# Kernel optimization log

Measured on AMD Instinct MI355X. Metric: run time of the kernel, lower is better.

## Reference

```python
import jax, jax.numpy as jnp
import numpy as np

B, S, V, E, H = 256, 256, 128, 512, 512
D1, D2, NT, NE = 1024, 512, 12, 5
BN_EPS = 1e-5


def setup_inputs() -> dict:
    key = jax.random.key(0)
    ks = jax.random.split(key, 12)
    p = lambda k, shape: jax.random.normal(k, shape, jnp.float32) * 0.05
    return dict(
        smiles=jax.random.randint(ks[0], (B, S), 0, V),
        emb=p(ks[1], (V, E)),
        W_ih0=p(ks[2], (3 * H, E)), W_hh0=p(ks[3], (3 * H, H)),
        b_ih0=jnp.zeros(3 * H), b_hh0=jnp.zeros(3 * H),
        W_ih1=p(ks[4], (3 * H, H)), W_hh1=p(ks[5], (3 * H, H)),
        b_ih1=jnp.zeros(3 * H), b_hh1=jnp.zeros(3 * H),
        Wd1=p(ks[6], (D1, H)), bd1=jnp.zeros(D1), g1=jnp.ones(D1), beta1=jnp.zeros(D1),
        Wd2=p(ks[7], (D2, D1)), bd2=jnp.zeros(D2), g2=jnp.ones(D2), beta2=jnp.zeros(D2),
        We=p(ks[8], (NE, NT, D2)), be=jnp.zeros((NE, NT)),
    )


def _gru_layer(x, W_ih, W_hh, b_ih, b_hh):
    """x: [B,S,Din]. Returns (h_T [B,H], seq [B,S,H]). Torch GRUCell math."""
    xi = jnp.einsum('bsd,gd->bsg', x, W_ih) + b_ih  # precompute input gates [B,S,3H]
    h0 = jnp.zeros((x.shape[0], W_hh.shape[0] // 3), x.dtype)

    def step(h, xi_t):
        hh = h @ W_hh.T + b_hh
        xr, xz, xn = jnp.split(xi_t, 3, axis=-1)
        hr, hz, hn = jnp.split(hh, 3, axis=-1)
        r = jax.nn.sigmoid(xr + hr)
        z = jax.nn.sigmoid(xz + hz)
        n = jnp.tanh(xn + r * hn)
        h_new = (1.0 - z) * n + z * h
        return h_new, h_new

    hT, hs = jax.lax.scan(step, h0, jnp.swapaxes(xi, 0, 1))
    return hT, jnp.swapaxes(hs, 0, 1)


def _bn(x, g, b):
    m = x.mean(0)
    v = x.var(0)
    return g * (x - m) * jax.lax.rsqrt(v + BN_EPS) + b


def reference(smiles, emb, W_ih0, W_hh0, b_ih0, b_hh0, W_ih1, W_hh1, b_ih1, b_hh1,
              Wd1, bd1, g1, beta1, Wd2, bd2, g2, beta2, We, be):
    x = emb[smiles]                                   # [B,S,E]
    _, seq = _gru_layer(x, W_ih0, W_hh0, b_ih0, b_hh0)  # [B,S,H]
    hT, _ = _gru_layer(seq, W_ih1, W_hh1, b_ih1, b_hh1)  # final hidden [B,H]
    h = jax.nn.relu(_bn(hT @ Wd1.T + bd1, g1, beta1))   # dense_0: Linear->BN->ReLU
    h = jax.nn.relu(_bn(h @ Wd2.T + bd2, g2, beta2))    # dense_1
    scores = jnp.einsum('bd,etd->bet', h, We) + be      # [B,NE,NT]
    return jax.nn.sigmoid(scores.mean(axis=1))          # ensemble 'score': sigmoid(mean)
```

## Files before the change

kernel.cpp:

```cpp
#include <hip/hip_runtime.h>
#include <stdint.h>

#define WS_TABLE0   0
#define WS_WHH0B    786432
#define WS_WIH1B    2359296
#define WS_WHH1B    3932160
#define WS_WD1B     5505024
#define WS_WD2B     6553600
#define WS_WM       7602176
#define WS_BM       7626752
#define WS_H0B      7627008
#define WS_H1B      8151296
#define WS_Y1       8675584
#define WS_X1B      9724160
#define WS_Y2       10248448
#define WS_X2B      10772736
#define WS_BAR      11034880

typedef __attribute__((ext_vector_type(8))) short bf16x8;
typedef __attribute__((ext_vector_type(4))) float f32x4;

__device__ __forceinline__ unsigned short f2bf(float f) {
  uint32_t u = __builtin_bit_cast(uint32_t, f);
  u += 0x7fffu + ((u >> 16) & 1u);
  return (unsigned short)(u >> 16);
}
__device__ __forceinline__ float bf2f(unsigned short s) {
  uint32_t u = ((uint32_t)s) << 16;
  return __builtin_bit_cast(float, u);
}
__device__ __forceinline__ float sigf(float x) { return 1.f / (1.f + __expf(-x)); }
__device__ __forceinline__ float tanhs(float x) {
  x = fminf(fmaxf(x, -10.f), 10.f);
  float e = __expf(2.f * x);
  return (e - 1.f) / (e + 1.f);
}

__device__ __forceinline__ unsigned long long pack4(float a, float b, float c, float d) {
  return (unsigned long long)f2bf(a) | ((unsigned long long)f2bf(b) << 16) |
         ((unsigned long long)f2bf(c) << 32) | ((unsigned long long)f2bf(d) << 48);
}

__device__ __forceinline__ void st_wt64(unsigned long long* p, unsigned long long v) {
  __hip_atomic_store(p, v, __ATOMIC_RELAXED, __HIP_MEMORY_SCOPE_AGENT);
}

__device__ __forceinline__ void gbar(int* bar, int expected) {
  __syncthreads();
  if (threadIdx.x == 0) {
    __threadfence();
    int g0 = __hip_atomic_load(bar + 1, __ATOMIC_RELAXED, __HIP_MEMORY_SCOPE_AGENT);
    int a = __hip_atomic_fetch_add(bar, 1, __ATOMIC_ACQ_REL, __HIP_MEMORY_SCOPE_AGENT);
    if (a == expected - 1) {
      __hip_atomic_store(bar, 0, __ATOMIC_RELAXED, __HIP_MEMORY_SCOPE_AGENT);
      __hip_atomic_fetch_add(bar + 1, 1, __ATOMIC_RELEASE, __HIP_MEMORY_SCOPE_AGENT);
    } else {
      while (__hip_atomic_load(bar + 1, __ATOMIC_RELAXED, __HIP_MEMORY_SCOPE_AGENT) == g0) {
        __builtin_amdgcn_s_sleep(1);
      }
    }
    __threadfence();
  }
  __syncthreads();
}

__global__ void k_zero(uint4* p, int n16) {
  int i = blockIdx.x * 256 + threadIdx.x;
  if (i < n16) p[i] = make_uint4(0u, 0u, 0u, 0u);
}

__global__ void k_cvt(const float* __restrict__ src, unsigned short* __restrict__ dst, int n) {
  int i = (blockIdx.x * 256 + threadIdx.x) * 4;
  if (i < n) {
    float4 v = *(const float4*)(src + i);
    dst[i + 0] = f2bf(v.x);
    dst[i + 1] = f2bf(v.y);
    dst[i + 2] = f2bf(v.z);
    dst[i + 3] = f2bf(v.w);
  }
}

__global__ void k_table(const float* __restrict__ emb, const float* __restrict__ Wih0,
                        const float* __restrict__ bih0, float* __restrict__ table) {
  __shared__ float e[512];
  int v = blockIdx.x;
  for (int i = threadIdx.x; i < 512; i += 256) e[i] = emb[v * 512 + i];
  __syncthreads();
  for (int cidx = threadIdx.x; cidx < 1536; cidx += 256) {
    const float* w = Wih0 + (size_t)cidx * 512;
    float s = 0.f;
    #pragma unroll 4
    for (int k = 0; k < 512; k += 4) {
      float4 w4 = *(const float4*)(w + k);
      s += w4.x * e[k] + w4.y * e[k + 1] + w4.z * e[k + 2] + w4.w * e[k + 3];
    }
    table[(size_t)v * 1536 + cidx] = s + bih0[cidx];
  }
}

__global__ void k_wm(const float* __restrict__ We, const float* __restrict__ be,
                     float* __restrict__ Wm, float* __restrict__ bm) {
  int i = blockIdx.x * 256 + threadIdx.x;
  if (i < 12 * 512) {
    int t = i / 512, d = i % 512;
    float s = 0.f;
    for (int e = 0; e < 5; ++e) s += We[((size_t)e * 12 + t) * 512 + d];
    Wm[i] = s * 0.2f;
  }
  if (i < 12) {
    float s = 0.f;
    for (int e = 0; e < 5; ++e) s += be[e * 12 + i];
    bm[i] = s * 0.2f;
  }
}

__global__ void __launch_bounds__(256, 1) k_main(
    const int* __restrict__ smiles,
    const float* __restrict__ bhh0,
    const float* __restrict__ bih1,
    const float* __restrict__ bhh1,
    const float* __restrict__ bd1,
    const float* __restrict__ gam1,
    const float* __restrict__ bet1,
    const float* __restrict__ bd2,
    const float* __restrict__ gam2,
    const float* __restrict__ bet2,
    char* __restrict__ ws,
    float* __restrict__ out) {
  extern __shared__ char lds[];
  const int tid = threadIdx.x, bid = blockIdx.x;
  const int lane = tid & 63, wave = tid >> 6;
  const int grp = bid & 7, member = bid >> 3;
  const int hc = member * 16;
  const int l15 = lane & 15, l4 = lane >> 4;

  const float* table0 = (const float*)(ws + WS_TABLE0);
  const unsigned short* Whh0b = (const unsigned short*)(ws + WS_WHH0B);
  const unsigned short* Wih1b = (const unsigned short*)(ws + WS_WIH1B);
  const unsigned short* Whh1b = (const unsigned short*)(ws + WS_WHH1B);
  const unsigned short* Wd1b = (const unsigned short*)(ws + WS_WD1B);
  const unsigned short* Wd2b = (const unsigned short*)(ws + WS_WD2B);
  const float* Wm = (const float*)(ws + WS_WM);
  const float* bm = (const float*)(ws + WS_BM);
  unsigned short* h0b = (unsigned short*)(ws + WS_H0B);
  unsigned short* h1b = (unsigned short*)(ws + WS_H1B);
  float* Y1 = (float*)(ws + WS_Y1);
  unsigned short* X1b = (unsigned short*)(ws + WS_X1B);
  float* Y2 = (float*)(ws + WS_Y2);
  unsigned short* X2b = (unsigned short*)(ws + WS_X2B);
  int* ecnt = (int*)(ws + WS_BAR) + grp * 64;
  int* barall = (int*)(ws + WS_BAR + 2048);

  float* accS = (float*)(lds + 147456);

  for (int u = tid; u < 3 * 48 * 64; u += 256) {
    int mat = u / (48 * 64);
    int rem = u - mat * (48 * 64);
    int r = rem >> 6, c16 = rem & 63;
    const unsigned short* src = (mat == 0) ? Whh0b : (mat == 1) ? Wih1b : Whh1b;
    int grow = (r >> 4) * 512 + hc + (r & 15);
    uint4 v = *(const uint4*)(src + (size_t)grow * 512 + c16 * 8);
    int off = mat * 49152 + r * 1024 + ((c16 * 16) ^ ((r & 7) << 4));
    *(uint4*)(lds + off) = v;
  }
  __syncthreads();

  const int c4 = hc + 4 * l4;
  const f32x4 bh0r4 = *(const f32x4*)(bhh0 + c4);
  const f32x4 bh0z4 = *(const f32x4*)(bhh0 + 512 + c4);
  const f32x4 bh0n4 = *(const f32x4*)(bhh0 + 1024 + c4);
  const f32x4 b1r4 = *(const f32x4*)(bih1 + c4) + *(const f32x4*)(bhh1 + c4);
  const f32x4 b1z4 = *(const f32x4*)(bih1 + 512 + c4) + *(const f32x4*)(bhh1 + 512 + c4);
  const f32x4 b1xn4 = *(const f32x4*)(bih1 + 1024 + c4);
  const f32x4 b1hn4 = *(const f32x4*)(bhh1 + 1024 + c4);
  const int swz = (l15 & 7) << 4;

  auto ldsB = [&](int mat, int gate, int kc) -> bf16x8 {
    int off = mat * 49152 + (gate * 16 + l15) * 1024 + ((((kc << 6) + (l4 << 4))) ^ swz);
    return *(const bf16x8*)(lds + off);
  };
  auto loadA = [&](const unsigned short* base, int kc) -> bf16x8 {
    return *(const bf16x8*)(base + (size_t)l15 * 512 + (kc << 5) + (l4 << 3));
  };

  float h0m[8], h1m[4];
  #pragma unroll
  for (int i = 0; i < 8; ++i) h0m[i] = 0.f;
  #pragma unroll
  for (int i = 0; i < 4; ++i) h1m[i] = 0.f;

  const int rowbase = grp * 32;
  const f32x4 z4 = {0.f, 0.f, 0.f, 0.f};

  f32x4 xg[2][3];
  int tokp[2];
  if (wave == 0) {
    #pragma unroll
    for (int mt = 0; mt < 2; ++mt) {
      int b = rowbase + mt * 16 + l15;
      int t0 = smiles[(size_t)b * 256 + 0];
      const float* tb = table0 + (size_t)t0 * 1536 + c4;
      xg[mt][0] = *(const f32x4*)(tb);
      xg[mt][1] = *(const f32x4*)(tb + 512);
      xg[mt][2] = *(const f32x4*)(tb + 1024);
      tokp[mt] = smiles[(size_t)b * 256 + 1];
    }
  }

  for (int s = 0; s <= 256; ++s) {
    const unsigned short* h0rd = h0b + (size_t)((s + 1) & 1) * 131072 + (size_t)rowbase * 512;
    const unsigned short* h1rd = h1b + (size_t)(s & 1) * 131072 + (size_t)rowbase * 512;

    f32x4 pr[2], pz[2], pxn[2], phn[2];
    pr[0] = z4; pr[1] = z4; pz[0] = z4; pz[1] = z4;
    pxn[0] = z4; pxn[1] = z4; phn[0] = z4; phn[1] = z4;

    if (wave == 0) {
      if (s < 256) {
        bf16x8 A0[16], A1[16];
        #pragma unroll
        for (int kc = 0; kc < 16; ++kc) {
          A0[kc] = loadA(h0rd, kc);
          A1[kc] = loadA(h0rd + 16 * 512, kc);
        }
        f32x4 acc[3][2];
        #pragma unroll
        for (int gi = 0; gi < 3; ++gi) { acc[gi][0] = z4; acc[gi][1] = z4; }
        #pragma unroll
        for (int kc = 0; kc < 16; ++kc) {
          #pragma unroll
          for (int gi = 0; gi < 3; ++gi) {
            bf16x8 bb = ldsB(0, gi, kc);
            acc[gi][0] = __builtin_amdgcn_mfma_f32_16x16x32_bf16(bb, A0[kc], acc[gi][0], 0, 0, 0);
            acc[gi][1] = __builtin_amdgcn_mfma_f32_16x16x32_bf16(bb, A1[kc], acc[gi][1], 0, 0, 0);
          }
        }
        unsigned short* h0wr = h0b + (size_t)(s & 1) * 131072;
        #pragma unroll
        for (int mt = 0; mt < 2; ++mt) {
          int b = rowbase + mt * 16 + l15;
          float hv[4];
          #pragma unroll
          for (int q = 0; q < 4; ++q) {
            float rr = sigf(xg[mt][0][q] + acc[0][mt][q] + bh0r4[q]);
            float zz = sigf(xg[mt][1][q] + acc[1][mt][q] + bh0z4[q]);
            float nn = tanhs(xg[mt][2][q] + rr * (acc[2][mt][q] + bh0n4[q]));
            hv[q] = (1.f - zz) * nn + zz * h0m[mt * 4 + q];
            h0m[mt * 4 + q] = hv[q];
          }
          st_wt64((unsigned long long*)(h0wr + (size_t)b * 512 + c4),
                  pack4(hv[0], hv[1], hv[2], hv[3]));
        }
        if (s + 1 < 256) {
          #pragma unroll
          for (int mt = 0; mt < 2; ++mt) {
            int b = rowbase + mt * 16 + l15;
            const float* tb = table0 + (size_t)tokp[mt] * 1536 + c4;
            xg[mt][0] = *(const f32x4*)(tb);
            xg[mt][1] = *(const f32x4*)(tb + 512);
            xg[mt][2] = *(const f32x4*)(tb + 1024);
            tokp[mt] = (s + 2 < 256) ? smiles[(size_t)b * 256 + s + 2] : 0;
          }
        }
      }
    } else {
      if (s >= 1) {
        const int wi = wave - 1;
        const int kc0 = (wi == 0) ? 0 : (wi == 1) ? 6 : 11;
        const int nk = (wi == 0) ? 6 : 5;
        bf16x8 X0[6], X1[6], Y0[6], Y1[6];
        #pragma unroll
        for (int i = 0; i < 6; ++i) {
          if (i < nk) {
            int kc = kc0 + i;
            X0[i] = loadA(h0rd, kc);
            X1[i] = loadA(h0rd + 16 * 512, kc);
            Y0[i] = loadA(h1rd, kc);
            Y1[i] = loadA(h1rd + 16 * 512, kc);
          }
        }
        #pragma unroll
        for (int i = 0; i < 6; ++i) {
          if (i < nk) {
            int kc = kc0 + i;
            bf16x8 bxr = ldsB(1, 0, kc), bxz = ldsB(1, 1, kc), bxn = ldsB(1, 2, kc);
            bf16x8 bhr = ldsB(2, 0, kc), bhz = ldsB(2, 1, kc), bhn = ldsB(2, 2, kc);
            pr[0] = __builtin_amdgcn_mfma_f32_16x16x32_bf16(bxr, X0[i], pr[0], 0, 0, 0);
            pr[0] = __builtin_amdgcn_mfma_f32_16x16x32_bf16(bhr, Y0[i], pr[0], 0, 0, 0);
            pr[1] = __builtin_amdgcn_mfma_f32_16x16x32_bf16(bxr, X1[i], pr[1], 0, 0, 0);
            pr[1] = __builtin_amdgcn_mfma_f32_16x16x32_bf16(bhr, Y1[i], pr[1], 0, 0, 0);
            pz[0] = __builtin_amdgcn_mfma_f32_16x16x32_bf16(bxz, X0[i], pz[0], 0, 0, 0);
            pz[0] = __builtin_amdgcn_mfma_f32_16x16x32_bf16(bhz, Y0[i], pz[0], 0, 0, 0);
            pz[1] = __builtin_amdgcn_mfma_f32_16x16x32_bf16(bxz, X1[i], pz[1], 0, 0, 0);
            pz[1] = __builtin_amdgcn_mfma_f32_16x16x32_bf16(bhz, Y1[i], pz[1], 0, 0, 0);
            pxn[0] = __builtin_amdgcn_mfma_f32_16x16x32_bf16(bxn, X0[i], pxn[0], 0, 0, 0);
            pxn[1] = __builtin_amdgcn_mfma_f32_16x16x32_bf16(bxn, X1[i], pxn[1], 0, 0, 0);
            phn[0] = __builtin_amdgcn_mfma_f32_16x16x32_bf16(bhn, Y0[i], phn[0], 0, 0, 0);
            phn[1] = __builtin_amdgcn_mfma_f32_16x16x32_bf16(bhn, Y1[i], phn[1], 0, 0, 0);
          }
        }
      }
    }

    #pragma unroll
    for (int r = 0; r < 3; ++r) {
      __syncthreads();
      if (wave >= 1 && s >= 1) {
        const int wi = wave - 1;
        #pragma unroll
        for (int j = 0; j < 8; ++j) {
          if (j % 3 == (wi + r) % 3) {
            const int gk = j >> 1, mt = j & 1;
            f32x4 v = (gk == 0) ? pr[mt] : (gk == 1) ? pz[mt] : (gk == 2) ? pxn[mt] : phn[mt];
            float* dstp = accS + j * 272;
            #pragma unroll
            for (int q = 0; q < 4; ++q) {
              int idx = (4 * l4 + q) * 17 + l15;
              if (r == 0) dstp[idx] = v[q];
              else dstp[idx] += v[q];
            }
          }
        }
      }
    }
    __syncthreads();
    if ((wave == 1 || wave == 2) && s >= 1) {
      const int mt = wave - 1;
      unsigned short* h1wr = h1b + (size_t)((s + 1) & 1) * 131072;
      int b = rowbase + mt * 16 + l15;
      float hv[4];
      #pragma unroll
      for (int q = 0; q < 4; ++q) {
        int idx = (4 * l4 + q) * 17 + l15;
        float rr = sigf(accS[(0 * 2 + mt) * 272 + idx] + b1r4[q]);
        float zz = sigf(accS[(1 * 2 + mt) * 272 + idx] + b1z4[q]);
        float nn = tanhs(accS[(2 * 2 + mt) * 272 + idx] + b1xn4[q] +
                         rr * (accS[(3 * 2 + mt) * 272 + idx] + b1hn4[q]));
        hv[q] = (1.f - zz) * nn + zz * h1m[q];
        h1m[q] = hv[q];
      }
      st_wt64((unsigned long long*)(h1wr + (size_t)b * 512 + c4),
              pack4(hv[0], hv[1], hv[2], hv[3]));
    }

    asm volatile("s_waitcnt vmcnt(0)" ::: "memory");
    __syncthreads();
    if (tid == 0) {
      __hip_atomic_fetch_add(ecnt, 1, __ATOMIC_RELAXED, __HIP_MEMORY_SCOPE_AGENT);
      while (__hip_atomic_load(ecnt, __ATOMIC_RELAXED, __HIP_MEMORY_SCOPE_AGENT) < 32 * (s + 1)) {
      }
    }
    if (wave == 0) __builtin_amdgcn_fence(__ATOMIC_ACQUIRE, "agent");
    __syncthreads();
  }

  gbar(barall, 256);

  {
    const int mi = bid & 15, ni = bid >> 4;
    const unsigned short* A = h1b + 131072 + (size_t)(16 * mi) * 512;
    const int colb = 64 * ni + 16 * wave;
    f32x4 acc = z4;
    #pragma unroll 4
    for (int kc = 0; kc < 16; ++kc) {
      bf16x8 a = loadA(A, kc);
      bf16x8 bb = *(const bf16x8*)(Wd1b + (size_t)(colb + l15) * 512 + (kc << 5) + (l4 << 3));
      acc = __builtin_amdgcn_mfma_f32_16x16x32_bf16(a, bb, acc, 0, 0, 0);
    }
    #pragma unroll
    for (int q = 0; q < 4; ++q) {
      int row = 16 * mi + 4 * l4 + q, col = colb + l15;
      Y1[(size_t)row * 1024 + col] = acc[q] + bd1[col];
    }
  }
  gbar(barall, 256);

  {
    float* red = (float*)lds;
    for (int cc = 0; cc < 4; ++cc) {
      int col = bid * 4 + cc;
      float x = Y1[(size_t)tid * 1024 + col];
      red[tid] = x; __syncthreads();
      for (int st = 128; st > 0; st >>= 1) { if (tid < st) red[tid] += red[tid + st]; __syncthreads(); }
      float mean = red[0] * (1.f / 256.f); __syncthreads();
      float d = x - mean;
      red[tid] = d * d; __syncthreads();
      for (int st = 128; st > 0; st >>= 1) { if (tid < st) red[tid] += red[tid + st]; __syncthreads(); }
      float var = red[0] * (1.f / 256.f); __syncthreads();
      float xn = gam1[col] * d * rsqrtf(var + 1e-5f) + bet1[col];
      X1b[(size_t)tid * 1024 + col] = f2bf(fmaxf(xn, 0.f));
    }
  }
  gbar(barall, 256);

  {
    const int mi = bid & 15, ni = bid >> 4;
    if (wave < 2) {
      const unsigned short* A = X1b + (size_t)(16 * mi) * 1024;
      const int colb = 32 * ni + 16 * wave;
      f32x4 acc = z4;
      #pragma unroll 4
      for (int kc = 0; kc < 32; ++kc) {
        bf16x8 a = *(const bf16x8*)(A + (size_t)l15 * 1024 + (kc << 5) + (l4 << 3));
        bf16x8 bb = *(const bf16x8*)(Wd2b + (size_t)(colb + l15) * 1024 + (kc << 5) + (l4 << 3));
        acc = __builtin_amdgcn_mfma_f32_16x16x32_bf16(a, bb, acc, 0, 0, 0);
      }
      #pragma unroll
      for (int q = 0; q < 4; ++q) {
        int row = 16 * mi + 4 * l4 + q, col = colb + l15;
        Y2[(size_t)row * 512 + col] = acc[q] + bd2[col];
      }
    }
  }
  gbar(barall, 256);

  {
    float* red = (float*)lds;
    for (int cc = 0; cc < 2; ++cc) {
      int col = bid * 2 + cc;
      float x = Y2[(size_t)tid * 512 + col];
      red[tid] = x; __syncthreads();
      for (int st = 128; st > 0; st >>= 1) { if (tid < st) red[tid] += red[tid + st]; __syncthreads(); }
      float mean = red[0] * (1.f / 256.f); __syncthreads();
      float d = x - mean;
      red[tid] = d * d; __syncthreads();
      for (int st = 128; st > 0; st >>= 1) { if (tid < st) red[tid] += red[tid + st]; __syncthreads(); }
      float var = red[0] * (1.f / 256.f); __syncthreads();
      float xn = gam2[col] * d * rsqrtf(var + 1e-5f) + bet2[col];
      X2b[(size_t)tid * 512 + col] = f2bf(fmaxf(xn, 0.f));
    }
  }
  gbar(barall, 256);

  {
    const int b = bid;
    float xa = bf2f(X2b[(size_t)b * 512 + tid]);
    float xb2 = bf2f(X2b[(size_t)b * 512 + 256 + tid]);
    float* red = (float*)lds;
    for (int t = 0; t < 12; ++t) {
      float p = xa * Wm[t * 512 + tid] + xb2 * Wm[t * 512 + 256 + tid];
      red[tid] = p; __syncthreads();
      for (int st = 128; st > 0; st >>= 1) { if (tid < st) red[tid] += red[tid + st]; __syncthreads(); }
      if (tid == 0) out[b * 12 + t] = sigf(red[0] + bm[t]);
      __syncthreads();
    }
  }
}

extern "C" void kernel_launch(void* const* d_in, const int* in_sizes, int n_in,
                              void* d_out, int out_size, void* d_ws, size_t ws_size,
                              hipStream_t stream) {
  const int* smiles = (const int*)d_in[0];
  const float* emb = (const float*)d_in[1];
  const float* Wih0 = (const float*)d_in[2];
  const float* Whh0 = (const float*)d_in[3];
  const float* bih0 = (const float*)d_in[4];
  const float* bhh0 = (const float*)d_in[5];
  const float* Wih1 = (const float*)d_in[6];
  const float* Whh1 = (const float*)d_in[7];
  const float* bih1 = (const float*)d_in[8];
  const float* bhh1 = (const float*)d_in[9];
  const float* Wd1 = (const float*)d_in[10];
  const float* bd1 = (const float*)d_in[11];
  const float* g1 = (const float*)d_in[12];
  const float* be1 = (const float*)d_in[13];
  const float* Wd2 = (const float*)d_in[14];
  const float* bd2 = (const float*)d_in[15];
  const float* g2 = (const float*)d_in[16];
  const float* be2 = (const float*)d_in[17];
  const float* We = (const float*)d_in[18];
  const float* be = (const float*)d_in[19];
  char* ws = (char*)d_ws;
  float* out = (float*)d_out;

  k_zero<<<256, 256, 0, stream>>>((uint4*)(ws + WS_H0B), 65536);
  k_zero<<<1, 256, 0, stream>>>((uint4*)(ws + WS_BAR), 256);
  k_cvt<<<768, 256, 0, stream>>>(Whh0, (unsigned short*)(ws + WS_WHH0B), 786432);
  k_cvt<<<768, 256, 0, stream>>>(Wih1, (unsigned short*)(ws + WS_WIH1B), 786432);
  k_cvt<<<768, 256, 0, stream>>>(Whh1, (unsigned short*)(ws + WS_WHH1B), 786432);
  k_cvt<<<512, 256, 0, stream>>>(Wd1, (unsigned short*)(ws + WS_WD1B), 524288);
  k_cvt<<<512, 256, 0, stream>>>(Wd2, (unsigned short*)(ws + WS_WD2B), 524288);
  k_table<<<128, 256, 0, stream>>>(emb, Wih0, bih0, (float*)(ws + WS_TABLE0));
  k_wm<<<24, 256, 0, stream>>>(We, be, (float*)(ws + WS_WM), (float*)(ws + WS_BM));

  const int LDS_BYTES = 156160;
  hipFuncSetAttribute((const void*)k_main, hipFuncAttributeMaxDynamicSharedMemorySize, LDS_BYTES);
  k_main<<<256, 256, LDS_BYTES, stream>>>(smiles, bhh0, bih1, bhh1, bd1, g1, be1,
                                          bd2, g2, be2, ws, out);
}
```

Measured before the change: 3.037 ms.

## Split layer-1 gates by wave and replace counter barrier with per-block flags

Layer-1 GRU work is repartitioned so each of waves 1-3 computes one whole gate over the full K range, rather than splitting K across waves. This removes the three-round LDS reduction of partial sums, and wave 3 now finishes the cell update using the r and z values written to LDS by waves 1 and 2. The group barrier's single shared atomic counter is replaced by per-member flag stores, with 32 threads each polling one flag. The trade is more global loads per wave (each reads all 16 K-chunks of both hidden states), the cell update now runs serially on one wave, and the flag loop moves the spin-wait after the acquire fence.

```diff
diff --git a/kernel.cpp b/kernel.cpp
--- a/kernel.cpp
+++ b/kernel.cpp
@@ -148,7 +148,7 @@
   unsigned short* X1b = (unsigned short*)(ws + WS_X1B);
   float* Y2 = (float*)(ws + WS_Y2);
   unsigned short* X2b = (unsigned short*)(ws + WS_X2B);
-  int* ecnt = (int*)(ws + WS_BAR) + grp * 64;
+  int* flags = (int*)(ws + WS_BAR) + grp * 32;
   int* barall = (int*)(ws + WS_BAR + 2048);
 
   float* accS = (float*)(lds + 147456);
@@ -183,11 +183,14 @@
     return *(const bf16x8*)(base + (size_t)l15 * 512 + (kc << 5) + (l4 << 3));
   };
 
-  float h0m[8], h1m[4];
+  float h0m[8];
+  float h1m[2][4];
   #pragma unroll
   for (int i = 0; i < 8; ++i) h0m[i] = 0.f;
   #pragma unroll
-  for (int i = 0; i < 4; ++i) h1m[i] = 0.f;
+  for (int mt = 0; mt < 2; ++mt)
+    #pragma unroll
+    for (int q = 0; q < 4; ++q) h1m[mt][q] = 0.f;
 
   const int rowbase = grp * 32;
   const f32x4 z4 = {0.f, 0.f, 0.f, 0.f};
@@ -211,9 +214,8 @@
     const unsigned short* h0rd = h0b + (size_t)((s + 1) & 1) * 131072 + (size_t)rowbase * 512;
     const unsigned short* h1rd = h1b + (size_t)(s & 1) * 131072 + (size_t)rowbase * 512;
 
-    f32x4 pr[2], pz[2], pxn[2], phn[2];
-    pr[0] = z4; pr[1] = z4; pz[0] = z4; pz[1] = z4;
-    pxn[0] = z4; pxn[1] = z4; phn[0] = z4; phn[1] = z4;
+    f32x4 accP[2] = {z4, z4};
+    f32x4 accQ[2] = {z4, z4};
 
     if (wave == 0) {
       if (s < 256) {
@@ -265,92 +267,80 @@
       }
     } else {
       if (s >= 1) {
-        const int wi = wave - 1;
-        const int kc0 = (wi == 0) ? 0 : (wi == 1) ? 6 : 11;
-        const int nk = (wi == 0) ? 6 : 5;
-        bf16x8 X0[6], X1[6], Y0[6], Y1[6];
+        const int g = (wave == 3) ? 2 : (wave - 1);
+        {
+          bf16x8 F0[16], F1[16];
+          #pragma unroll
+          for (int kc = 0; kc < 16; ++kc) {
+            F0[kc] = loadA(h0rd, kc);
+            F1[kc] = loadA(h0rd + 16 * 512, kc);
+          }
+          #pragma unroll
+          for (int kc = 0; kc < 16; ++kc) {
+            bf16x8 w = ldsB(1, g, kc);
+            accP[0] = __builtin_amdgcn_mfma_f32_16x16x32_bf16(w, F0[kc], accP[0], 0, 0, 0);
+            accP[1] = __builtin_amdgcn_mfma_f32_16x16x32_bf16(w, F1[kc], accP[1], 0, 0, 0);
+          }
+        }
+        {
+          bf16x8 F0[16], F1[16];
+          #pragma unroll
+          for (int kc = 0; kc < 16; ++kc) {
+            F0[kc] = loadA(h1rd, kc);
+            F1[kc] = loadA(h1rd + 16 * 512, kc);
+          }
+          #pragma unroll
+          for (int kc = 0; kc < 16; ++kc) {
+            bf16x8 w = ldsB(2, g, kc);
+            if (wave == 3) {
+              accQ[0] = __builtin_amdgcn_mfma_f32_16x16x32_bf16(w, F0[kc], accQ[0], 0, 0, 0);
+              accQ[1] = __builtin_amdgcn_mfma_f32_16x16x32_bf16(w, F1[kc], accQ[1], 0, 0, 0);
+            } else {
+              accP[0] = __builtin_amdgcn_mfma_f32_16x16x32_bf16(w, F0[kc], accP[0], 0, 0, 0);
+              accP[1] = __builtin_amdgcn_mfma_f32_16x16x32_bf16(w, F1[kc], accP[1], 0, 0, 0);
+            }
+          }
+        }
+        if (wave == 1 || wave == 2) {
+          float* dst = accS + (wave - 1) * 512;
+          *(f32x4*)(dst + 0 * 256 + lane * 4) = accP[0];
+          *(f32x4*)(dst + 1 * 256 + lane * 4) = accP[1];
+        }
+      }
+    }
+
+    __syncthreads();
+
+    if (wave == 3 && s >= 1) {
+      unsigned short* h1wr = h1b + (size_t)((s + 1) & 1) * 131072;
+      #pragma unroll
+      for (int mt = 0; mt < 2; ++mt) {
+        f32x4 rr4 = *(const f32x4*)(accS + 0 * 512 + mt * 256 + lane * 4);
+        f32x4 zz4 = *(const f32x4*)(accS + 1 * 512 + mt * 256 + lane * 4);
+        int b = rowbase + mt * 16 + l15;
+        float hv[4];
         #pragma unroll
-        for (int i = 0; i < 6; ++i) {
-          if (i < nk) {
-            int kc = kc0 + i;
-            X0[i] = loadA(h0rd, kc);
-            X1[i] = loadA(h0rd + 16 * 512, kc);
-            Y0[i] = loadA(h1rd, kc);
-            Y1[i] = loadA(h1rd + 16 * 512, kc);
-          }
-        }
-        #pragma unroll
-        for (int i = 0; i < 6; ++i) {
-          if (i < nk) {
-            int kc = kc0 + i;
-            bf16x8 bxr = ldsB(1, 0, kc), bxz = ldsB(1, 1, kc), bxn = ldsB(1, 2, kc);
-            bf16x8 bhr = ldsB(2, 0, kc), bhz = ldsB(2, 1, kc), bhn = ldsB(2, 2, kc);
-            pr[0] = __builtin_amdgcn_mfma_f32_16x16x32_bf16(bxr, X0[i], pr[0], 0, 0, 0);
-            pr[0] = __builtin_amdgcn_mfma_f32_16x16x32_bf16(bhr, Y0[i], pr[0], 0, 0, 0);
-            pr[1] = __builtin_amdgcn_mfma_f32_16x16x32_bf16(bxr, X1[i], pr[1], 0, 0, 0);
-            pr[1] = __builtin_amdgcn_mfma_f32_16x16x32_bf16(bhr, Y1[i], pr[1], 0, 0, 0);
-            pz[0] = __builtin_amdgcn_mfma_f32_16x16x32_bf16(bxz, X0[i], pz[0], 0, 0, 0);
-            pz[0] = __builtin_amdgcn_mfma_f32_16x16x32_bf16(bhz, Y0[i], pz[0], 0, 0, 0);
-            pz[1] = __builtin_amdgcn_mfma_f32_16x16x32_bf16(bxz, X1[i], pz[1], 0, 0, 0);
-            pz[1] = __builtin_amdgcn_mfma_f32_16x16x32_bf16(bhz, Y1[i], pz[1], 0, 0, 0);
-            pxn[0] = __builtin_amdgcn_mfma_f32_16x16x32_bf16(bxn, X0[i], pxn[0], 0, 0, 0);
-            pxn[1] = __builtin_amdgcn_mfma_f32_16x16x32_bf16(bxn, X1[i], pxn[1], 0, 0, 0);
-            phn[0] = __builtin_amdgcn_mfma_f32_16x16x32_bf16(bhn, Y0[i], phn[0], 0, 0, 0);
-            phn[1] = __builtin_amdgcn_mfma_f32_16x16x32_bf16(bhn, Y1[i], phn[1], 0, 0, 0);
-          }
-        }
-      }
-    }
-
-    #pragma unroll
-    for (int r = 0; r < 3; ++r) {
-      __syncthreads();
-      if (wave >= 1 && s >= 1) {
-        const int wi = wave - 1;
-        #pragma unroll
-        for (int j = 0; j < 8; ++j) {
-          if (j % 3 == (wi + r) % 3) {
-            const int gk = j >> 1, mt = j & 1;
-            f32x4 v = (gk == 0) ? pr[mt] : (gk == 1) ? pz[mt] : (gk == 2) ? pxn[mt] : phn[mt];
-            float* dstp = accS + j * 272;
-            #pragma unroll
-            for (int q = 0; q < 4; ++q) {
-              int idx = (4 * l4 + q) * 17 + l15;
-              if (r == 0) dstp[idx] = v[q];
-              else dstp[idx] += v[q];
-            }
-          }
-        }
-      }
-    }
-    __syncthreads();
-    if ((wave == 1 || wave == 2) && s >= 1) {
-      const int mt = wave - 1;
-      unsigned short* h1wr = h1b + (size_t)((s + 1) & 1) * 131072;
-      int b = rowbase + mt * 16 + l15;
-      float hv[4];
-      #pragma unroll
-      for (int q = 0; q < 4; ++q) {
-        int idx = (4 * l4 + q) * 17 + l15;
-        float rr = sigf(accS[(0 * 2 + mt) * 272 + idx] + b1r4[q]);
-        float zz = sigf(accS[(1 * 2 + mt) * 272 + idx] + b1z4[q]);
-        float nn = tanhs(accS[(2 * 2 + mt) * 272 + idx] + b1xn4[q] +
-                         rr * (accS[(3 * 2 + mt) * 272 + idx] + b1hn4[q]));
-        hv[q] = (1.f - zz) * nn + zz * h1m[q];
-        h1m[q] = hv[q];
-      }
-      st_wt64((unsigned long long*)(h1wr + (size_t)b * 512 + c4),
-              pack4(hv[0], hv[1], hv[2], hv[3]));
+        for (int q = 0; q < 4; ++q) {
+          float rr = sigf(rr4[q] + b1r4[q]);
+          float zz = sigf(zz4[q] + b1z4[q]);
+          float nn = tanhs(accP[mt][q] + b1xn4[q] + rr * (accQ[mt][q] + b1hn4[q]));
+          hv[q] = (1.f - zz) * nn + zz * h1m[mt][q];
+          h1m[mt][q] = hv[q];
+        }
+        st_wt64((unsigned long long*)(h1wr + (size_t)b * 512 + c4),
+                pack4(hv[0], hv[1], hv[2], hv[3]));
+      }
     }
 
     asm volatile("s_waitcnt vmcnt(0)" ::: "memory");
     __syncthreads();
-    if (tid == 0) {
-      __hip_atomic_fetch_add(ecnt, 1, __ATOMIC_RELAXED, __HIP_MEMORY_SCOPE_AGENT);
-      while (__hip_atomic_load(ecnt, __ATOMIC_RELAXED, __HIP_MEMORY_SCOPE_AGENT) < 32 * (s + 1)) {
-      }
-    }
+    if (tid == 0)
+      __hip_atomic_store(&flags[member], s + 1, __ATOMIC_RELAXED, __HIP_MEMORY_SCOPE_AGENT);
     if (wave == 0) __builtin_amdgcn_fence(__ATOMIC_ACQUIRE, "agent");
+    if (tid < 32) {
+      while (__hip_atomic_load(&flags[tid], __ATOMIC_RELAXED, __HIP_MEMORY_SCOPE_AGENT) < s + 1) {
+      }
+    }
     __syncthreads();
   }
 
```

New measurement: 3.337 ms. 9.9% more time.
